# Optimization experiments

Hardware: AMD Instinct MI355X
Metric: run time of the kernel (lower is better)

The kernel has to match this reference:

```python
import jax, jax.numpy as jnp
import numpy as np

N, E, F_IN, HID, H, G = 50000, 800000, 128, 128, 4, 64
D = HID // H  # per-head dim = 32


def setup_inputs() -> dict:
    key = jax.random.key(0)
    ks = jax.random.split(key, 24)
    s = 0.05
    x = jax.random.normal(ks[0], (N, F_IN), dtype=jnp.float32)
    edge_index = jax.random.randint(ks[1], (2, E), 0, N, dtype=jnp.int64)
    batch = jnp.sort(jax.random.randint(ks[2], (N,), 0, G, dtype=jnp.int64))
    p = {}
    # layer 1: in F_IN -> H*D, layer 2: in HID -> H*D; each conv has q,k,v,skip linears (bias=True)
    names = ['Wq1', 'Wk1', 'Wv1', 'Ws1', 'Wq2', 'Wk2', 'Wv2', 'Ws2']
    dims = [(F_IN, HID)] * 4 + [(HID, HID)] * 4
    for i, (nm, dm) in enumerate(zip(names, dims)):
        p[nm] = jax.random.normal(ks[3 + 2 * i], dm, dtype=jnp.float32) * s
        p['b' + nm[1:]] = jax.random.normal(ks[4 + 2 * i], (dm[1],), dtype=jnp.float32) * s
    p['Wfc'] = jax.random.normal(ks[20], (HID, 1), dtype=jnp.float32) * s
    p['bfc'] = jax.random.normal(ks[21], (1,), dtype=jnp.float32) * s
    return {'x': x, 'edge_index': edge_index, 'batch': batch, **p}


def transformer_conv(x, edge_index, Wq, bq, Wk, bk, Wv, bv, Ws, bs):
    src, dst = edge_index[0], edge_index[1]  # messages flow src -> dst
    q = (x @ Wq + bq).reshape(-1, H, D)[dst]          # [E,H,D]
    k = (x @ Wk + bk).reshape(-1, H, D)[src]          # [E,H,D]
    v = (x @ Wv + bv).reshape(-1, H, D)[src]          # [E,H,D]
    logits = jnp.einsum('ehd,ehd->eh', q, k) / jnp.sqrt(jnp.float32(D))  # [E,H]
    m = jax.ops.segment_max(logits, dst, num_segments=N)                 # [N,H]
    e = jnp.exp(logits - m[dst])
    s = jax.ops.segment_sum(e, dst, num_segments=N)                      # [N,H]
    alpha = e / s[dst]
    agg = jax.ops.segment_sum(alpha[..., None] * v, dst, num_segments=N)  # [N,H,D]
    return agg.reshape(-1, HID) + (x @ Ws + bs)


def reference(x, edge_index, batch, Wq1, bq1, Wk1, bk1, Wv1, bv1, Ws1, bs1,
              Wq2, bq2, Wk2, bk2, Wv2, bv2, Ws2, bs2, Wfc, bfc):
    h = jax.nn.relu(transformer_conv(x, edge_index, Wq1, bq1, Wk1, bk1, Wv1, bv1, Ws1, bs1))
    h = jax.nn.relu(transformer_conv(h, edge_index, Wq2, bq2, Wk2, bk2, Wv2, bv2, Ws2, bs2))
    sums = jax.ops.segment_sum(h, batch, num_segments=G)                 # [G,HID]
    cnt = jax.ops.segment_sum(jnp.ones((h.shape[0],), h.dtype), batch, num_segments=G)
    pooled = sums / jnp.maximum(cnt, 1.0)[:, None]
    return (pooled @ Wfc + bfc).squeeze(-1)
```

## Files before the change

### kernel.cpp

```cpp
#include <hip/hip_runtime.h>
#include <hip/hip_bf16.h>
#include <math.h>

#define HID 128

typedef __attribute__((ext_vector_type(8))) short short8;
typedef __attribute__((ext_vector_type(4))) short short4v;
typedef __attribute__((ext_vector_type(4))) float f32x4;
typedef __attribute__((ext_vector_type(2))) float f32x2;
typedef __attribute__((ext_vector_type(4))) unsigned short ushort4v;
typedef __attribute__((ext_vector_type(2))) unsigned short ushort2v;

static inline size_t align256(size_t x){ return (x + 255) & ~(size_t)255; }

__device__ inline float bf2f(unsigned short h) {
  union { unsigned u; float f; } uf; uf.u = ((unsigned)h) << 16; return uf.f;
}
__device__ inline unsigned short f2bf(float f) {
  union { float f; unsigned u; } uf; uf.f = f;
  unsigned r = uf.u + 0x7fff + ((uf.u >> 16) & 1);
  return (unsigned short)(r >> 16);
}

__device__ inline float dpp_rsum16(float x) {
  int v;
  v = __builtin_amdgcn_update_dpp(0, __float_as_int(x), 0xB1, 0xF, 0xF, true);
  x += __int_as_float(v);
  v = __builtin_amdgcn_update_dpp(0, __float_as_int(x), 0x4E, 0xF, 0xF, true);
  x += __int_as_float(v);
  v = __builtin_amdgcn_update_dpp(0, __float_as_int(x), 0x124, 0xF, 0xF, true);
  x += __int_as_float(v);
  v = __builtin_amdgcn_update_dpp(0, __float_as_int(x), 0x128, 0xF, 0xF, true);
  x += __int_as_float(v);
  return x;
}

__global__ __launch_bounds__(256) void k_wprep(
    const float* W0, const float* W1, const float* W2, const float* W3,
    const float* W4, const float* W5, const float* W6, const float* W7,
    const float* b0, const float* b1, const float* b2, const float* b3,
    const float* b4, const float* b5, const float* b6, const float* b7,
    unsigned short* Wcat, float* Bcat)
{
  __shared__ float tl[32][33];
  const float* Ws[8] = {W0, W1, W2, W3, W4, W5, W6, W7};
  const float* bs[8] = {b0, b1, b2, b3, b4, b5, b6, b7};
  int m = blockIdx.x >> 4, tile = blockIdx.x & 15;
  int tr = (tile >> 2) * 32, tc = (tile & 3) * 32;
  int tx = threadIdx.x & 31, ty = threadIdx.x >> 5;
  const float* Wm = Ws[m];
  #pragma unroll
  for (int r = 0; r < 32; r += 8) tl[ty + r][tx] = Wm[(tr + ty + r) * 128 + tc + tx];
  __syncthreads();
  #pragma unroll
  for (int r = 0; r < 32; r += 8)
    Wcat[m * 16384 + (tc + ty + r) * 128 + tr + tx] = f2bf(tl[tx][ty + r]);
  if (tile == 0 && threadIdx.x < 128) Bcat[m * 128 + threadIdx.x] = bs[m][threadIdx.x];
}

__global__ void k_hist(const int* __restrict__ dst, int* __restrict__ deg, int e) {
  for (int i = blockIdx.x * blockDim.x + threadIdx.x; i < e; i += gridDim.x * blockDim.x)
    atomicAdd(&deg[dst[i]], 1);
}

__global__ void k_scan_a(const int* __restrict__ deg, int* __restrict__ rowptr,
                         int* __restrict__ bsum, int n) {
  __shared__ int tmp[512];
  int t = threadIdx.x, i = blockIdx.x * 512 + t;
  int v = (i < n) ? deg[i] : 0;
  tmp[t] = v;
  __syncthreads();
  for (int off = 1; off < 512; off <<= 1) {
    int u = (t >= off) ? tmp[t - off] : 0;
    __syncthreads();
    tmp[t] += u;
    __syncthreads();
  }
  if (i < n) rowptr[i] = tmp[t] - v;
  if (t == 511) bsum[blockIdx.x] = tmp[t];
}

__global__ void k_scan_b(int* bsum, int nb) {
  __shared__ int tmp[512];
  int t = threadIdx.x;
  int v = (t < nb) ? bsum[t] : 0;
  tmp[t] = v;
  __syncthreads();
  for (int off = 1; off < 512; off <<= 1) {
    int u = (t >= off) ? tmp[t - off] : 0;
    __syncthreads();
    tmp[t] += u;
    __syncthreads();
  }
  if (t < nb) bsum[t] = tmp[t] - v;
}

__global__ void k_scan_c(int* __restrict__ rowptr, int* __restrict__ cursor,
                         const int* __restrict__ bsum, int n, int e) {
  int i = blockIdx.x * 512 + threadIdx.x;
  if (i < n) { int v = rowptr[i] + bsum[blockIdx.x]; rowptr[i] = v; cursor[i] = v; }
  if (i == 0) rowptr[n] = e;
}

__global__ void k_scatter(const int* __restrict__ srcA, const int* __restrict__ dstA,
                          int* __restrict__ cursor, int* __restrict__ csrc, int e) {
  for (int i = blockIdx.x * blockDim.x + threadIdx.x; i < e; i += gridDim.x * blockDim.x) {
    int pos = atomicAdd(&cursor[dstA[i]], 1);
    csrc[pos] = srcA[i];
  }
}

template<int ABF16>
__global__ __launch_bounds__(256, 2) void k_qkvs(
    const void* __restrict__ Ain, const unsigned short* __restrict__ Wl,
    const float* __restrict__ Bl, unsigned short* __restrict__ Qb,
    unsigned short* __restrict__ KVb, float* __restrict__ Sb, int n)
{
  __shared__ unsigned short sA[128 * 128];
  __shared__ unsigned short sW[128 * 128];
  const int tid = threadIdx.x;
  const int rb = blockIdx.x * 128;

  if (ABF16) {
    const unsigned short* A = (const unsigned short*)Ain;
    #pragma unroll
    for (int it = 0; it < 8; ++it) {
      int q = tid + it * 256;
      int row = q >> 4, ch = q & 15;
      int gr = rb + row;
      short8 h = {0,0,0,0,0,0,0,0};
      if (gr < n) h = *reinterpret_cast<const short8*>(A + (size_t)gr * HID + ch * 8);
      *reinterpret_cast<short8*>(&sA[row * 128 + ((ch ^ (row & 7)) << 3)]) = h;
    }
  } else {
    const float* A = (const float*)Ain;
    #pragma unroll
    for (int it = 0; it < 16; ++it) {
      int q = tid + it * 256;
      int row = q >> 5, c4 = (q & 31) * 4;
      int gr = rb + row;
      f32x4 a = {0.f, 0.f, 0.f, 0.f};
      if (gr < n) a = *reinterpret_cast<const f32x4*>(A + (size_t)gr * HID + c4);
      short4v h;
      h.x = (short)f2bf(a.x); h.y = (short)f2bf(a.y);
      h.z = (short)f2bf(a.z); h.w = (short)f2bf(a.w);
      int eloff = row * 128 + (((c4 >> 3) ^ (row & 7)) << 3) + (c4 & 7);
      *reinterpret_cast<short4v*>(&sA[eloff]) = h;
    }
  }

  const int lane = tid & 63;
  const int wv = tid >> 6;

  auto stageW = [&](int y) {
    const unsigned short* Wy = Wl + (size_t)y * 16384;
    #pragma unroll
    for (int it = 0; it < 8; ++it) {
      int q = tid + it * 256;
      int c = q >> 4, ch = q & 15;
      short8 w = *reinterpret_cast<const short8*>(Wy + c * 128 + ch * 8);
      *reinterpret_cast<short8*>(&sW[c * 128 + ((ch ^ (c & 7)) << 3)]) = w;
    }
  };

  stageW(0);
  __syncthreads();

  short8 af[4][2];
  #pragma unroll
  for (int ks = 0; ks < 4; ++ks) {
    int ch = ks * 4 + (lane >> 4);
    #pragma unroll
    for (int nf = 0; nf < 2; ++nf) {
      int row = wv * 32 + nf * 16 + (lane & 15);
      af[ks][nf] = *reinterpret_cast<const short8*>(&sA[row * 128 + ((ch ^ (row & 7)) << 3)]);
    }
  }

  f32x4 acc[8][2];
  auto compute = [&]() {
    #pragma unroll
    for (int mf = 0; mf < 8; ++mf)
      #pragma unroll
      for (int nf = 0; nf < 2; ++nf)
        acc[mf][nf] = (f32x4){0.f, 0.f, 0.f, 0.f};
    #pragma unroll
    for (int ks = 0; ks < 4; ++ks) {
      int ch = ks * 4 + (lane >> 4);
      short8 wf[8];
      #pragma unroll
      for (int mf = 0; mf < 8; ++mf) {
        int wc = mf * 16 + (lane & 15);
        wf[mf] = *reinterpret_cast<const short8*>(&sW[wc * 128 + ((ch ^ (wc & 7)) << 3)]);
      }
      #pragma unroll
      for (int mf = 0; mf < 8; ++mf)
        #pragma unroll
        for (int nf = 0; nf < 2; ++nf)
          acc[mf][nf] = __builtin_amdgcn_mfma_f32_16x16x32_bf16(wf[mf], af[ks][nf], acc[mf][nf], 0, 0, 0);
    }
  };

  compute();
  #pragma unroll
  for (int nf = 0; nf < 2; ++nf) {
    int gr = rb + wv * 32 + nf * 16 + (lane & 15);
    if (gr >= n) continue;
    #pragma unroll
    for (int mf = 0; mf < 8; ++mf) {
      int c0 = mf * 16 + ((lane >> 4) << 2);
      f32x4 b = *reinterpret_cast<const f32x4*>(Bl + 0 * 128 + c0);
      f32x4 v = acc[mf][nf];
      short4v h;
      h.x = (short)f2bf(v.x + b.x); h.y = (short)f2bf(v.y + b.y);
      h.z = (short)f2bf(v.z + b.z); h.w = (short)f2bf(v.w + b.w);
      *reinterpret_cast<short4v*>(Qb + (size_t)gr * HID + c0) = h;
    }
  }

  __syncthreads();
  stageW(3);
  __syncthreads();
  compute();
  #pragma unroll
  for (int nf = 0; nf < 2; ++nf) {
    int gr = rb + wv * 32 + nf * 16 + (lane & 15);
    if (gr >= n) continue;
    #pragma unroll
    for (int mf = 0; mf < 8; ++mf) {
      int c0 = mf * 16 + ((lane >> 4) << 2);
      f32x4 b = *reinterpret_cast<const f32x4*>(Bl + 3 * 128 + c0);
      f32x4 v = acc[mf][nf];
      v.x += b.x; v.y += b.y; v.z += b.z; v.w += b.w;
      *reinterpret_cast<f32x4*>(Sb + (size_t)gr * HID + c0) = v;
    }
  }

  __syncthreads();
  stageW(1);
  __syncthreads();
  compute();
  f32x4 kacc[8][2];
  #pragma unroll
  for (int mf = 0; mf < 8; ++mf)
    #pragma unroll
    for (int nf = 0; nf < 2; ++nf) kacc[mf][nf] = acc[mf][nf];

  __syncthreads();
  stageW(2);
  __syncthreads();
  compute();
  #pragma unroll
  for (int nf = 0; nf < 2; ++nf) {
    int gr = rb + wv * 32 + nf * 16 + (lane & 15);
    if (gr >= n) continue;
    #pragma unroll
    for (int mf = 0; mf < 8; ++mf) {
      int c0 = mf * 16 + ((lane >> 4) << 2);
      f32x4 bk = *reinterpret_cast<const f32x4*>(Bl + 1 * 128 + c0);
      f32x4 bv = *reinterpret_cast<const f32x4*>(Bl + 2 * 128 + c0);
      f32x4 kv = kacc[mf][nf], vv = acc[mf][nf];
      short8 h;
      h[0] = (short)f2bf(kv.x + bk.x); h[1] = (short)f2bf(kv.y + bk.y);
      h[2] = (short)f2bf(vv.x + bv.x); h[3] = (short)f2bf(vv.y + bv.y);
      h[4] = (short)f2bf(kv.z + bk.z); h[5] = (short)f2bf(kv.w + bk.w);
      h[6] = (short)f2bf(vv.z + bv.z); h[7] = (short)f2bf(vv.w + bv.w);
      *reinterpret_cast<short8*>(KVb + (size_t)gr * 256 + 2 * c0) = h;
    }
  }
}

__global__ __launch_bounds__(256) void k_attn2(
    const unsigned short* __restrict__ Qb, const unsigned short* __restrict__ KVb,
    const float* __restrict__ Sb, const int* __restrict__ rowptr,
    const int* __restrict__ csrc, unsigned short* __restrict__ Hout, int n)
{
  int wid = blockIdx.x * 4 + (threadIdx.x >> 6);
  if (wid >= n) return;
  int lane = threadIdx.x & 63;
  ushort2v qv = *reinterpret_cast<const ushort2v*>(Qb + (size_t)wid * HID + 2 * lane);
  const float sc = 0.17677669529663687f;
  float q0 = bf2f(qv.x) * sc, q1 = bf2f(qv.y) * sc;
  int e0 = rowptr[wid], deg = rowptr[wid + 1] - e0;
  const int* cp = csrc + e0;
  float m = -INFINITY, s = 0.f, a0 = 0.f, a1 = 0.f;

  auto LD = [&](int i) -> ushort4v {
    return *reinterpret_cast<const ushort4v*>(KVb + (size_t)cp[i] * 256 + 4 * lane);
  };
  auto proc = [&](ushort4v kv) {
    float d = q0 * bf2f(kv.x) + q1 * bf2f(kv.y);
    float lg = dpp_rsum16(d);
    float nm = fmaxf(m, lg);
    float cc = __expf(m - nm);
    float p  = __expf(lg - nm);
    s  = s * cc + p;
    a0 = a0 * cc + p * bf2f(kv.z);
    a1 = a1 * cc + p * bf2f(kv.w);
    m = nm;
  };

  ushort4v z = {0, 0, 0, 0};
  ushort4v b0 = z, b1 = z, b2 = z, b3 = z;
  if (deg > 0) b0 = LD(0);
  if (deg > 1) b1 = LD(1);
  if (deg > 2) b2 = LD(2);
  if (deg > 3) b3 = LD(3);
  for (int j = 0; j < deg; j += 4) {
    ushort4v n0 = z, n1 = z, n2 = z, n3 = z;
    if (j + 4 < deg) n0 = LD(j + 4);
    if (j + 5 < deg) n1 = LD(j + 5);
    if (j + 6 < deg) n2 = LD(j + 6);
    if (j + 7 < deg) n3 = LD(j + 7);
    proc(b0);
    if (j + 1 < deg) proc(b1);
    if (j + 2 < deg) proc(b2);
    if (j + 3 < deg) proc(b3);
    b0 = n0; b1 = n1; b2 = n2; b3 = n3;
  }
  float inv = (s > 0.f) ? 1.f / s : 0.f;
  f32x2 sv = *reinterpret_cast<const f32x2*>(Sb + (size_t)wid * HID + 2 * lane);
  ushort2v h;
  h.x = f2bf(fmaxf(a0 * inv + sv.x, 0.f));
  h.y = f2bf(fmaxf(a1 * inv + sv.y, 0.f));
  *reinterpret_cast<ushort2v*>(Hout + (size_t)wid * HID + 2 * lane) = h;
}

__global__ void k_pool(const unsigned short* __restrict__ Hin, const int* __restrict__ batch,
                       float* __restrict__ psum, float* __restrict__ pcnt, int n) {
  int t = threadIdx.x;
  int chunk = (n + gridDim.x - 1) / gridDim.x;
  int n0 = blockIdx.x * chunk, n1 = min(n, n0 + chunk);
  if (n0 >= n1) return;
  int curg = batch[n0];
  float acc = 0.f; int c = 0;
  for (int i = n0; i < n1; ++i) {
    int g = batch[i];
    if (g != curg) {
      atomicAdd(&psum[curg * HID + t], acc);
      if (t == 0) atomicAdd(&pcnt[curg], (float)c);
      acc = 0.f; c = 0; curg = g;
    }
    acc += bf2f(Hin[(size_t)i * HID + t]); ++c;
  }
  atomicAdd(&psum[curg * HID + t], acc);
  if (t == 0) atomicAdd(&pcnt[curg], (float)c);
}

__global__ void k_fc(const float* __restrict__ psum, const float* __restrict__ pcnt,
                     const float* __restrict__ Wfc, const float* __restrict__ bfc,
                     float* __restrict__ out) {
  __shared__ float red[2];
  int g = blockIdx.x, t = threadIdx.x;
  float v = psum[g * HID + t] * Wfc[t];
  #pragma unroll
  for (int off = 32; off >= 1; off >>= 1) v += __shfl_xor(v, off);
  if ((t & 63) == 0) red[t >> 6] = v;
  __syncthreads();
  if (t == 0) out[g] = (red[0] + red[1]) / fmaxf(pcnt[g], 1.f) + bfc[0];
}

extern "C" void kernel_launch(void* const* d_in, const int* in_sizes, int n_in,
                              void* d_out, int out_size, void* d_ws, size_t ws_size,
                              hipStream_t stream)
{
  const float* x   = (const float*)d_in[0];
  const int*   ei  = (const int*)d_in[1];
  const int*   bat = (const int*)d_in[2];
  const float *Wq1 = (const float*)d_in[3],  *bq1 = (const float*)d_in[4];
  const float *Wk1 = (const float*)d_in[5],  *bk1 = (const float*)d_in[6];
  const float *Wv1 = (const float*)d_in[7],  *bv1 = (const float*)d_in[8];
  const float *Ws1 = (const float*)d_in[9],  *bs1 = (const float*)d_in[10];
  const float *Wq2 = (const float*)d_in[11], *bq2 = (const float*)d_in[12];
  const float *Wk2 = (const float*)d_in[13], *bk2 = (const float*)d_in[14];
  const float *Wv2 = (const float*)d_in[15], *bv2 = (const float*)d_in[16];
  const float *Ws2 = (const float*)d_in[17], *bs2 = (const float*)d_in[18];
  const float *Wfc = (const float*)d_in[19], *bfc = (const float*)d_in[20];
  float* out = (float*)d_out;

  const int N = in_sizes[0] / HID;
  const int E = in_sizes[1] / 2;
  const int G = 64;

  char* p = (char*)d_ws;
  auto alloc = [&](size_t bytes) -> char* { char* r = p; p += align256(bytes); return r; };
  unsigned short* Qb  = (unsigned short*)alloc((size_t)N * HID * 2);
  unsigned short* KVb = (unsigned short*)alloc((size_t)N * 256 * 2);
  float* Sb   = (float*)alloc((size_t)N * HID * 4);
  unsigned short* Hb  = (unsigned short*)alloc((size_t)N * HID * 2);
  unsigned short* H2b = (unsigned short*)alloc((size_t)N * HID * 2);
  unsigned short* Wcat = (unsigned short*)alloc((size_t)8 * 128 * 128 * 2);
  float* Bcat = (float*)alloc((size_t)8 * 128 * 4);
  int* rowptr = (int*)alloc((size_t)(N + 1) * sizeof(int));
  int* cursor = (int*)alloc((size_t)N * sizeof(int));
  int* deg    = (int*)alloc((size_t)N * sizeof(int));
  int* bsum   = (int*)alloc(4096);
  int* csrc   = (int*)alloc((size_t)E * sizeof(int));
  float* psum = (float*)alloc((size_t)G * HID * sizeof(float));
  float* pcnt = (float*)alloc((size_t)G * sizeof(float));

  const int* esrc = ei;
  const int* edst = ei + E;

  hipMemsetAsync(deg, 0, (size_t)N * sizeof(int), stream);
  hipMemsetAsync(psum, 0, (size_t)G * HID * sizeof(float), stream);
  hipMemsetAsync(pcnt, 0, (size_t)G * sizeof(float), stream);

  k_wprep<<<128, 256, 0, stream>>>(Wq1, Wk1, Wv1, Ws1, Wq2, Wk2, Wv2, Ws2,
                                   bq1, bk1, bv1, bs1, bq2, bk2, bv2, bs2, Wcat, Bcat);

  k_hist<<<512, 256, 0, stream>>>(edst, deg, E);
  int SB = (N + 511) / 512;
  k_scan_a<<<SB, 512, 0, stream>>>(deg, rowptr, bsum, N);
  k_scan_b<<<1, 512, 0, stream>>>(bsum, SB);
  k_scan_c<<<SB, 512, 0, stream>>>(rowptr, cursor, bsum, N, E);
  k_scatter<<<512, 256, 0, stream>>>(esrc, edst, cursor, csrc, E);

  int QB = (N + 127) / 128;
  k_qkvs<0><<<QB, 256, 0, stream>>>(x, Wcat, Bcat, Qb, KVb, Sb, N);
  k_attn2<<<(N + 3) / 4, 256, 0, stream>>>(Qb, KVb, Sb, rowptr, csrc, Hb, N);
  k_qkvs<1><<<QB, 256, 0, stream>>>(Hb, Wcat + 4 * 16384, Bcat + 512, Qb, KVb, Sb, N);
  k_attn2<<<(N + 3) / 4, 256, 0, stream>>>(Qb, KVb, Sb, rowptr, csrc, H2b, N);
  k_pool<<<1024, 128, 0, stream>>>(H2b, bat, psum, pcnt, N);
  k_fc<<<G, 128, 0, stream>>>(psum, pcnt, Wfc, bfc, out);
}
```

Baseline: 453.9 us.

## Halve GEMM row tile, pre-scale edge indices, and use lazy-rescale exp2 softmax

The QKVS projection kernel now processes 64 rows per block instead of 128, so it launches twice as many blocks with half the A tile in shared memory and fewer accumulators per wave. The CSR source indices are pre-shifted to byte offsets, which removes the multiply from the attention gather. The attention kernel folds log2(e) into the query scale and uses exp2. It only rescales the running max when some lane's logit exceeds it by a threshold, which skips most rescale exps. The neighbour loop is restructured into full groups of four plus a tail, which removes per-element bounds checks. Trade-offs: smaller GEMM tiles stage W more often per row, and the shifted indices overflow int range if N grows beyond about 4M.

Measured after the change: 410.6 us. -9.6%, faster.

```diff
diff --git a/kernel.cpp b/kernel.cpp
--- a/kernel.cpp
+++ b/kernel.cpp
@@ -106,7 +106,7 @@
                           int* __restrict__ cursor, int* __restrict__ csrc, int e) {
   for (int i = blockIdx.x * blockDim.x + threadIdx.x; i < e; i += gridDim.x * blockDim.x) {
     int pos = atomicAdd(&cursor[dstA[i]], 1);
-    csrc[pos] = srcA[i];
+    csrc[pos] = srcA[i] << 9;
   }
 }
 
@@ -116,15 +116,15 @@
     const float* __restrict__ Bl, unsigned short* __restrict__ Qb,
     unsigned short* __restrict__ KVb, float* __restrict__ Sb, int n)
 {
-  __shared__ unsigned short sA[128 * 128];
+  __shared__ unsigned short sA[64 * 128];
   __shared__ unsigned short sW[128 * 128];
   const int tid = threadIdx.x;
-  const int rb = blockIdx.x * 128;
+  const int rb = blockIdx.x * 64;
 
   if (ABF16) {
     const unsigned short* A = (const unsigned short*)Ain;
     #pragma unroll
-    for (int it = 0; it < 8; ++it) {
+    for (int it = 0; it < 4; ++it) {
       int q = tid + it * 256;
       int row = q >> 4, ch = q & 15;
       int gr = rb + row;
@@ -135,7 +135,7 @@
   } else {
     const float* A = (const float*)Ain;
     #pragma unroll
-    for (int it = 0; it < 16; ++it) {
+    for (int it = 0; it < 8; ++it) {
       int q = tid + it * 256;
       int row = q >> 5, c4 = (q & 31) * 4;
       int gr = rb + row;
@@ -166,24 +166,18 @@
   stageW(0);
   __syncthreads();
 
-  short8 af[4][2];
+  short8 af[4];
   #pragma unroll
   for (int ks = 0; ks < 4; ++ks) {
     int ch = ks * 4 + (lane >> 4);
-    #pragma unroll
-    for (int nf = 0; nf < 2; ++nf) {
-      int row = wv * 32 + nf * 16 + (lane & 15);
-      af[ks][nf] = *reinterpret_cast<const short8*>(&sA[row * 128 + ((ch ^ (row & 7)) << 3)]);
-    }
-  }
-
-  f32x4 acc[8][2];
+    int row = wv * 16 + (lane & 15);
+    af[ks] = *reinterpret_cast<const short8*>(&sA[row * 128 + ((ch ^ (row & 7)) << 3)]);
+  }
+
+  f32x4 acc[8];
   auto compute = [&]() {
     #pragma unroll
-    for (int mf = 0; mf < 8; ++mf)
-      #pragma unroll
-      for (int nf = 0; nf < 2; ++nf)
-        acc[mf][nf] = (f32x4){0.f, 0.f, 0.f, 0.f};
+    for (int mf = 0; mf < 8; ++mf) acc[mf] = (f32x4){0.f, 0.f, 0.f, 0.f};
     #pragma unroll
     for (int ks = 0; ks < 4; ++ks) {
       int ch = ks * 4 + (lane >> 4);
@@ -195,22 +189,20 @@
       }
       #pragma unroll
       for (int mf = 0; mf < 8; ++mf)
-        #pragma unroll
-        for (int nf = 0; nf < 2; ++nf)
-          acc[mf][nf] = __builtin_amdgcn_mfma_f32_16x16x32_bf16(wf[mf], af[ks][nf], acc[mf][nf], 0, 0, 0);
+        acc[mf] = __builtin_amdgcn_mfma_f32_16x16x32_bf16(wf[mf], af[ks], acc[mf], 0, 0, 0);
     }
   };
 
+  const int gr = rb + wv * 16 + (lane & 15);
+  const int cbase = (lane >> 4) << 2;
+
   compute();
-  #pragma unroll
-  for (int nf = 0; nf < 2; ++nf) {
-    int gr = rb + wv * 32 + nf * 16 + (lane & 15);
-    if (gr >= n) continue;
+  if (gr < n) {
     #pragma unroll
     for (int mf = 0; mf < 8; ++mf) {
-      int c0 = mf * 16 + ((lane >> 4) << 2);
+      int c0 = mf * 16 + cbase;
       f32x4 b = *reinterpret_cast<const f32x4*>(Bl + 0 * 128 + c0);
-      f32x4 v = acc[mf][nf];
+      f32x4 v = acc[mf];
       short4v h;
       h.x = (short)f2bf(v.x + b.x); h.y = (short)f2bf(v.y + b.y);
       h.z = (short)f2bf(v.z + b.z); h.w = (short)f2bf(v.w + b.w);
@@ -222,15 +214,12 @@
   stageW(3);
   __syncthreads();
   compute();
-  #pragma unroll
-  for (int nf = 0; nf < 2; ++nf) {
-    int gr = rb + wv * 32 + nf * 16 + (lane & 15);
-    if (gr >= n) continue;
+  if (gr < n) {
     #pragma unroll
     for (int mf = 0; mf < 8; ++mf) {
-      int c0 = mf * 16 + ((lane >> 4) << 2);
+      int c0 = mf * 16 + cbase;
       f32x4 b = *reinterpret_cast<const f32x4*>(Bl + 3 * 128 + c0);
-      f32x4 v = acc[mf][nf];
+      f32x4 v = acc[mf];
       v.x += b.x; v.y += b.y; v.z += b.z; v.w += b.w;
       *reinterpret_cast<f32x4*>(Sb + (size_t)gr * HID + c0) = v;
     }
@@ -240,26 +229,21 @@
   stageW(1);
   __syncthreads();
   compute();
-  f32x4 kacc[8][2];
+  f32x4 kacc[8];
   #pragma unroll
-  for (int mf = 0; mf < 8; ++mf)
-    #pragma unroll
-    for (int nf = 0; nf < 2; ++nf) kacc[mf][nf] = acc[mf][nf];
+  for (int mf = 0; mf < 8; ++mf) kacc[mf] = acc[mf];
 
   __syncthreads();
   stageW(2);
   __syncthreads();
   compute();
-  #pragma unroll
-  for (int nf = 0; nf < 2; ++nf) {
-    int gr = rb + wv * 32 + nf * 16 + (lane & 15);
-    if (gr >= n) continue;
+  if (gr < n) {
     #pragma unroll
     for (int mf = 0; mf < 8; ++mf) {
-      int c0 = mf * 16 + ((lane >> 4) << 2);
+      int c0 = mf * 16 + cbase;
       f32x4 bk = *reinterpret_cast<const f32x4*>(Bl + 1 * 128 + c0);
       f32x4 bv = *reinterpret_cast<const f32x4*>(Bl + 2 * 128 + c0);
-      f32x4 kv = kacc[mf][nf], vv = acc[mf][nf];
+      f32x4 kv = kacc[mf], vv = acc[mf];
       short8 h;
       h[0] = (short)f2bf(kv.x + bk.x); h[1] = (short)f2bf(kv.y + bk.y);
       h[2] = (short)f2bf(vv.x + bv.x); h[3] = (short)f2bf(vv.y + bv.y);
@@ -279,45 +263,52 @@
   if (wid >= n) return;
   int lane = threadIdx.x & 63;
   ushort2v qv = *reinterpret_cast<const ushort2v*>(Qb + (size_t)wid * HID + 2 * lane);
-  const float sc = 0.17677669529663687f;
+  const float sc = 0.25503487f;
   float q0 = bf2f(qv.x) * sc, q1 = bf2f(qv.y) * sc;
   int e0 = rowptr[wid], deg = rowptr[wid + 1] - e0;
   const int* cp = csrc + e0;
+  const char* kvb = (const char*)KVb;
   float m = -INFINITY, s = 0.f, a0 = 0.f, a1 = 0.f;
 
   auto LD = [&](int i) -> ushort4v {
-    return *reinterpret_cast<const ushort4v*>(KVb + (size_t)cp[i] * 256 + 4 * lane);
+    return *reinterpret_cast<const ushort4v*>(kvb + (unsigned)cp[i] + lane * 8);
   };
   auto proc = [&](ushort4v kv) {
     float d = q0 * bf2f(kv.x) + q1 * bf2f(kv.y);
     float lg = dpp_rsum16(d);
-    float nm = fmaxf(m, lg);
-    float cc = __expf(m - nm);
-    float p  = __expf(lg - nm);
-    s  = s * cc + p;
-    a0 = a0 * cc + p * bf2f(kv.z);
-    a1 = a1 * cc + p * bf2f(kv.w);
-    m = nm;
+    if (!__all(lg <= m + 11.5f)) {
+      float nm = fmaxf(m, lg);
+      float cc = __builtin_amdgcn_exp2f(m - nm);
+      s *= cc; a0 *= cc; a1 *= cc; m = nm;
+    }
+    float p = __builtin_amdgcn_exp2f(lg - m);
+    s += p;
+    a0 = fmaf(p, bf2f(kv.z), a0);
+    a1 = fmaf(p, bf2f(kv.w), a1);
   };
 
-  ushort4v z = {0, 0, 0, 0};
-  ushort4v b0 = z, b1 = z, b2 = z, b3 = z;
-  if (deg > 0) b0 = LD(0);
-  if (deg > 1) b1 = LD(1);
-  if (deg > 2) b2 = LD(2);
-  if (deg > 3) b3 = LD(3);
-  for (int j = 0; j < deg; j += 4) {
-    ushort4v n0 = z, n1 = z, n2 = z, n3 = z;
-    if (j + 4 < deg) n0 = LD(j + 4);
-    if (j + 5 < deg) n1 = LD(j + 5);
-    if (j + 6 < deg) n2 = LD(j + 6);
-    if (j + 7 < deg) n3 = LD(j + 7);
-    proc(b0);
-    if (j + 1 < deg) proc(b1);
-    if (j + 2 < deg) proc(b2);
-    if (j + 3 < deg) proc(b3);
-    b0 = n0; b1 = n1; b2 = n2; b3 = n3;
-  }
+  int nq = deg >> 2, r = deg & 3;
+  if (nq) {
+    ushort4v b0 = LD(0), b1 = LD(1), b2 = LD(2), b3 = LD(3);
+    for (int q = 1; q < nq; ++q) {
+      int base = q * 4;
+      ushort4v n0 = LD(base), n1 = LD(base + 1), n2 = LD(base + 2), n3 = LD(base + 3);
+      proc(b0); proc(b1); proc(b2); proc(b3);
+      b0 = n0; b1 = n1; b2 = n2; b3 = n3;
+    }
+    int tb = nq * 4;
+    ushort4v t0, t1, t2;
+    if (r > 0) t0 = LD(tb);
+    if (r > 1) t1 = LD(tb + 1);
+    if (r > 2) t2 = LD(tb + 2);
+    proc(b0); proc(b1); proc(b2); proc(b3);
+    if (r > 0) proc(t0);
+    if (r > 1) proc(t1);
+    if (r > 2) proc(t2);
+  } else {
+    for (int i = 0; i < r; ++i) proc(LD(i));
+  }
+
   float inv = (s > 0.f) ? 1.f / s : 0.f;
   f32x2 sv = *reinterpret_cast<const f32x2*>(Sb + (size_t)wid * HID + 2 * lane);
   ushort2v h;
@@ -416,7 +407,7 @@
   k_scan_c<<<SB, 512, 0, stream>>>(rowptr, cursor, bsum, N, E);
   k_scatter<<<512, 256, 0, stream>>>(esrc, edst, cursor, csrc, E);
 
-  int QB = (N + 127) / 128;
+  int QB = (N + 63) / 64;
   k_qkvs<0><<<QB, 256, 0, stream>>>(x, Wcat, Bcat, Qb, KVb, Sb, N);
   k_attn2<<<(N + 3) / 4, 256, 0, stream>>>(Qb, KVb, Sb, rowptr, csrc, Hb, N);
   k_qkvs<1><<<QB, 256, 0, stream>>>(Hb, Wcat + 4 * 16384, Bcat + 512, Qb, KVb, Sb, N);
```
